# Optimization experiments

Hardware: AMD Instinct MI355X
Metric: run time of the kernel (lower is better)

Reference implementation:

```python
import jax, jax.numpy as jnp
import numpy as np
from math import comb

P, R, NC, SH = 2048, 32, 4, 3   # patches, resolution, degree+1 ctrl pts, max SH degree
N = P * R * R
NSH = (SH + 1) ** 2
EPS = 10.0


def _bernstein_basis():
    # Clamped knots [0]*(p+1)+[1]*(p+1) => B-spline basis == Bernstein polynomials.
    t = np.linspace(0.0, 1.0, R)
    bern = lambda p: np.stack([comb(p, k) * t**k * (1 - t)**(p - k) for k in range(p + 1)], -1)
    b3, b2, b1 = bern(3), bern(2), bern(1)
    db = 3.0 * (np.pad(b2, ((0, 0), (1, 0))) - np.pad(b2, ((0, 0), (0, 1))))
    ddb = 6.0 * (np.pad(b1, ((0, 0), (2, 0))) - 2.0 * np.pad(b1, ((0, 0), (1, 1))) + np.pad(b1, ((0, 0), (0, 2))))
    return b3.astype(np.float32), db.astype(np.float32), ddb.astype(np.float32)


def setup_inputs() -> dict:
    key = jax.random.key(0)
    ks = jax.random.split(key, 5)
    b, db, ddb = _bernstein_basis()
    tile = lambda a: jnp.asarray(np.broadcast_to(a, (P, R, NC)).copy())
    return {
        "control_points": jax.random.normal(ks[0], (P, NC, NC, 3), jnp.float32),
        "nurbs_weights": jax.random.uniform(ks[1], (P, NC, NC), jnp.float32, 0.5, 1.5),
        "sh_dc": jax.random.normal(ks[2], (P, NC, NC, 1, 3), jnp.float32),
        "sh_rest": jax.random.normal(ks[3], (P, NC, NC, NSH - 1, 3), jnp.float32) * 0.1,
        "scale_params": jax.random.uniform(ks[4], (P, 2), jnp.float32, 0.5, 1.5),
        "opacity": jnp.ones((N, 1), jnp.float32),
        "b_u": tile(b), "b_v": tile(b),
        "db_u": tile(db), "db_v": tile(db),
        "ddb_u": tile(ddb), "ddb_v": tile(ddb),
    }


def reference(control_points, nurbs_weights, sh_dc, sh_rest, scale_params, opacity,
              b_u, b_v, db_u, db_v, ddb_u, ddb_v):
    # NURBS rational denominator [P,R,R] -> [N,1]
    den = jnp.einsum('aik,ajl,akl->aij', b_u, b_v, nurbs_weights).reshape(-1, 1)
    den = jnp.where(den == 0, 1.0, den)
    wcp = control_points * nurbs_weights[..., None]        # weighted control points [P,4,4,3]
    surf = lambda Bu, Bv: jnp.einsum('aik,ajl,aklm->aijm', Bu, Bv, wcp).reshape(-1, 3) / den
    xyz = surf(b_u, b_v)
    dus = surf(db_u, b_v)
    dvs = surf(b_u, db_v)
    ddus = surf(ddb_u, b_v)
    ddvs = surf(b_u, ddb_v)

    # SH feature synthesis [N, 16, 3]
    sh_feat = jnp.concatenate([sh_dc, sh_rest], axis=-2).reshape(P, NC, NC, -1)
    shs = jnp.einsum('aik,ajl,aklm->aijm', b_u, b_v, sh_feat).reshape(-1, NSH, 3)

    # per-patch surface area (mean |du x dv| over the grid; param domain has unit area)
    cross = jnp.cross(dus, dvs)
    areas = jnp.linalg.norm(cross, axis=-1).reshape(P, R * R).mean(-1)          # [P]
    sp3 = jnp.concatenate([scale_params, jnp.full((P, 1), 1e-16, jnp.float32)], -1)
    scale_factors = jnp.repeat((areas[:, None] / R**2) * sp3, R * R, axis=0)    # [N,3]

    # torch uses F.normalize(..., p=1): L1 normalization
    normals = cross / jnp.maximum(jnp.abs(cross).sum(-1, keepdims=True), 1e-12)

    sx = (dus * dus).sum(-1) + EPS
    sy = (dvs * dvs).sum(-1) + EPS
    scaling_vec = jnp.stack([sx, sy, jnp.full_like(sx, EPS)], -1)
    curvature = jnp.stack([ddus.sum(-1), ddvs.sum(-1), jnp.ones_like(sx)], -1)
    # (sf*s).abs().sqrt().log() == 0.5*log|sf*s|
    scaling = 0.5 * jnp.log(jnp.abs(scale_factors * scaling_vec)) - jnp.log(jnp.abs(curvature) + EPS)

    # quaternion rotating up=[0,0,1] onto the (L2-unit) normal: q = normalize([1+dot, cross])
    n = normals / jnp.maximum(jnp.linalg.norm(normals, axis=-1, keepdims=True), 1e-12)
    w = 1.0 + n[:, 2:3]
    xyzq = jnp.stack([-n[:, 1], n[:, 0], jnp.zeros_like(n[:, 0])], -1)  # cross(up, n)
    q = jnp.concatenate([w, xyzq], -1)
    rotation = q / jnp.maximum(jnp.linalg.norm(q, axis=-1, keepdims=True), 1e-12)

    return (xyz, opacity, scaling, rotation, shs)
```

## Files before the change

### kernel.cpp

```cpp
#include <hip/hip_runtime.h>
#include <math.h>

#define NPATCH 2048
#define NPTS 1024
#define NTOT (NPATCH * NPTS)

using f4 = __attribute__((ext_vector_type(4))) float;

__device__ __forceinline__ void nt_store4(float* p, float a, float b, float c, float d) {
    f4 v = {a, b, c, d};
    __builtin_nontemporal_store(v, reinterpret_cast<f4*>(p));
}
__device__ __forceinline__ void nt_copy4(float* dst, const float* src) {
    f4 v = *reinterpret_cast<const f4*>(src);
    __builtin_nontemporal_store(v, reinterpret_cast<f4*>(dst));
}

__global__ __launch_bounds__(256) void area_kernel(
    const float* __restrict__ cp,
    const float* __restrict__ Wt,
    const float* __restrict__ b_u,
    const float* __restrict__ b_v,
    const float* __restrict__ db_u,
    const float* __restrict__ db_v,
    float* __restrict__ ws)
{
    const int a = blockIdx.x;
    const int t = threadIdx.x;

    __shared__ float s_W[16];
    __shared__ __align__(16) float s_wcp4[16][4];
    __shared__ __align__(16) float s_bu[32][4];
    __shared__ __align__(16) float s_bv[32][4];
    __shared__ __align__(16) float s_dbu[32][4];
    __shared__ __align__(16) float s_dbv[32][4];
    __shared__ __align__(16) float s_tB[128][4];
    __shared__ __align__(16) float s_tD[128][4];
    __shared__ __align__(16) float s_wB[128];
    __shared__ float s_red[4];

    if (t < 16) {
        const float w = Wt[a * 16 + t];
        s_W[t] = w;
        s_wcp4[t][0] = cp[a * 48 + t * 3 + 0] * w;
        s_wcp4[t][1] = cp[a * 48 + t * 3 + 1] * w;
        s_wcp4[t][2] = cp[a * 48 + t * 3 + 2] * w;
        s_wcp4[t][3] = 0.f;
    }
    if (t < 128) {
        s_bu [t >> 2][t & 3] = b_u [a * 128 + t];
        s_bv [t >> 2][t & 3] = b_v [a * 128 + t];
        s_dbu[t >> 2][t & 3] = db_u[a * 128 + t];
        s_dbv[t >> 2][t & 3] = db_v[a * 128 + t];
    }
    __syncthreads();

    if (t < 128) {
        const int i = t >> 2, l = t & 3;
        f4 acc = {0.f, 0.f, 0.f, 0.f};
        float wa = 0.f;
        #pragma unroll
        for (int k = 0; k < 4; ++k) {
            const float b = s_bu[i][k];
            acc += b * *reinterpret_cast<const f4*>(s_wcp4[k * 4 + l]);
            wa  += b * s_W[k * 4 + l];
        }
        *reinterpret_cast<f4*>(s_tB[t]) = acc;
        s_wB[t] = wa;
    } else {
        const int tt = t - 128;
        const int i = tt >> 2, l = tt & 3;
        f4 acc = {0.f, 0.f, 0.f, 0.f};
        #pragma unroll
        for (int k = 0; k < 4; ++k)
            acc += s_dbu[i][k] * *reinterpret_cast<const f4*>(s_wcp4[k * 4 + l]);
        *reinterpret_cast<f4*>(s_tD[tt]) = acc;
    }
    __syncthreads();

    const int j = t & 31;
    const f4 bv  = *reinterpret_cast<const f4*>(s_bv[j]);
    const f4 dbv = *reinterpret_cast<const f4*>(s_dbv[j]);

    float acc = 0.f;
    #pragma unroll
    for (int s2 = 0; s2 < 4; ++s2) {
        const int i = (t >> 5) + 8 * s2;
        const f4 tb0 = *reinterpret_cast<const f4*>(s_tB[i * 4 + 0]);
        const f4 tb1 = *reinterpret_cast<const f4*>(s_tB[i * 4 + 1]);
        const f4 tb2 = *reinterpret_cast<const f4*>(s_tB[i * 4 + 2]);
        const f4 tb3 = *reinterpret_cast<const f4*>(s_tB[i * 4 + 3]);
        const f4 td0 = *reinterpret_cast<const f4*>(s_tD[i * 4 + 0]);
        const f4 td1 = *reinterpret_cast<const f4*>(s_tD[i * 4 + 1]);
        const f4 td2 = *reinterpret_cast<const f4*>(s_tD[i * 4 + 2]);
        const f4 td3 = *reinterpret_cast<const f4*>(s_tD[i * 4 + 3]);
        const f4 wb  = *(reinterpret_cast<const f4*>(s_wB) + i);

        float den = bv.x * wb.x + bv.y * wb.y + bv.z * wb.z + bv.w * wb.w;
        if (den == 0.f) den = 1.f;
        const float inv = 1.0f / den;

        const f4 du = bv.x  * td0 + bv.y  * td1 + bv.z  * td2 + bv.w  * td3;
        const f4 dv = dbv.x * tb0 + dbv.y * tb1 + dbv.z * tb2 + dbv.w * tb3;

        const float cx = du.y * dv.z - du.z * dv.y;
        const float cy = du.z * dv.x - du.x * dv.z;
        const float cz = du.x * dv.y - du.y * dv.x;
        acc += sqrtf(cx * cx + cy * cy + cz * cz) * inv * inv;
    }

    #pragma unroll
    for (int off = 32; off > 0; off >>= 1)
        acc += __shfl_down(acc, off, 64);
    if ((t & 63) == 0) s_red[t >> 6] = acc;
    __syncthreads();
    if (t == 0) ws[a] = s_red[0] + s_red[1] + s_red[2] + s_red[3];
}

__global__ __launch_bounds__(256) void fused_kernel(
    const float* __restrict__ cp,
    const float* __restrict__ Wt,
    const float* __restrict__ sh_dc,
    const float* __restrict__ sh_rest,
    const float* __restrict__ spar,
    const float* __restrict__ opac,
    const float* __restrict__ b_u,
    const float* __restrict__ b_v,
    const float* __restrict__ db_u,
    const float* __restrict__ db_v,
    const float* __restrict__ ddb_u,
    const float* __restrict__ ddb_v,
    const float* __restrict__ ws,
    float* __restrict__ out)
{
    const int blk = blockIdx.x;
    const int a = blk >> 2, q = blk & 3;
    const int t = threadIdx.x;

    __shared__ float s_W[16];
    __shared__ __align__(16) float s_wcp4[16][4];
    __shared__ __align__(16) float g_bu[8][4];
    __shared__ __align__(16) float g_dbu[8][4];
    __shared__ __align__(16) float g_ddbu[8][4];
    __shared__ __align__(16) float g_bv[32][4];
    __shared__ __align__(16) float g_dbv[32][4];
    __shared__ __align__(16) float g_ddbv[32][4];
    __shared__ __align__(16) float s_tB[32][4];
    __shared__ __align__(16) float s_tD[32][4];
    __shared__ __align__(16) float s_tE[32][4];
    __shared__ __align__(16) float s_wB[32];
    __shared__ __align__(16) float s_sh[16][48];
    __shared__ __align__(16) float s_tmp[8 * 208];
    __shared__ __align__(16) float s_xyz[768];
    __shared__ __align__(16) float s_scl[768];

    if (t < 16) {
        const float w = Wt[a * 16 + t];
        s_W[t] = w;
        s_wcp4[t][0] = cp[a * 48 + t * 3 + 0] * w;
        s_wcp4[t][1] = cp[a * 48 + t * 3 + 1] * w;
        s_wcp4[t][2] = cp[a * 48 + t * 3 + 2] * w;
        s_wcp4[t][3] = 0.f;
    }
    if (t < 32) {
        g_bu  [t >> 2][t & 3] = b_u  [a * 128 + q * 32 + t];
        g_dbu [t >> 2][t & 3] = db_u [a * 128 + q * 32 + t];
        g_ddbu[t >> 2][t & 3] = ddb_u[a * 128 + q * 32 + t];
    }
    if (t < 128) {
        g_bv  [t >> 2][t & 3] = b_v  [a * 128 + t];
        g_dbv [t >> 2][t & 3] = db_v [a * 128 + t];
        g_ddbv[t >> 2][t & 3] = ddb_v[a * 128 + t];
    }
    for (int idx = t; idx < 768; idx += 256) {
        const int kl = idx / 48, c = idx - kl * 48;
        s_sh[kl][c] = (c < 3) ? sh_dc[a * 48 + kl * 3 + c]
                              : sh_rest[a * 720 + kl * 45 + (c - 3)];
    }
    __syncthreads();

    if (t < 32) {
        const int i = t >> 2, l = t & 3;
        f4 acc = {0.f, 0.f, 0.f, 0.f};
        float wa = 0.f;
        #pragma unroll
        for (int k = 0; k < 4; ++k) {
            const float b = g_bu[i][k];
            acc += b * *reinterpret_cast<const f4*>(s_wcp4[k * 4 + l]);
            wa  += b * s_W[k * 4 + l];
        }
        *reinterpret_cast<f4*>(s_tB[t]) = acc;
        s_wB[t] = wa;
    } else if (t < 64) {
        const int tt = t - 32, i = tt >> 2, l = tt & 3;
        f4 acc = {0.f, 0.f, 0.f, 0.f};
        #pragma unroll
        for (int k = 0; k < 4; ++k)
            acc += g_dbu[i][k] * *reinterpret_cast<const f4*>(s_wcp4[k * 4 + l]);
        *reinterpret_cast<f4*>(s_tD[tt]) = acc;
    } else if (t < 96) {
        const int tt = t - 64, i = tt >> 2, l = tt & 3;
        f4 acc = {0.f, 0.f, 0.f, 0.f};
        #pragma unroll
        for (int k = 0; k < 4; ++k)
            acc += g_ddbu[i][k] * *reinterpret_cast<const f4*>(s_wcp4[k * 4 + l]);
        *reinterpret_cast<f4*>(s_tE[tt]) = acc;
    }
    #pragma unroll
    for (int r = 0; r < 2; ++r) {
        const int e4 = t + r * 256;
        if (e4 < 384) {
            const int i = e4 / 48, rem = e4 - i * 48;
            const int l = rem / 12, cq = rem - l * 12;
            float ax = 0.f, ay = 0.f, az = 0.f, aw = 0.f;
            #pragma unroll
            for (int k = 0; k < 4; ++k) {
                const float w = g_bu[i][k];
                const float4 v = *reinterpret_cast<const float4*>(&s_sh[k * 4 + l][cq * 4]);
                ax += w * v.x; ay += w * v.y; az += w * v.z; aw += w * v.w;
            }
            *reinterpret_cast<float4*>(&s_tmp[i * 208 + l * 52 + cq * 4]) =
                make_float4(ax, ay, az, aw);
        }
    }
    __syncthreads();

    const long N3 = 3L * NTOT, N4 = 4L * NTOT, N7 = 7L * NTOT;
    const long n0 = (long)a * NPTS + q * 256;
    const long n  = n0 + t;

    {
        const int i = t >> 5, j = t & 31;
        const f4 bv   = *reinterpret_cast<const f4*>(g_bv[j]);
        const f4 dbv  = *reinterpret_cast<const f4*>(g_dbv[j]);
        const f4 ddbv = *reinterpret_cast<const f4*>(g_ddbv[j]);

        const f4 tb0 = *reinterpret_cast<const f4*>(s_tB[i * 4 + 0]);
        const f4 tb1 = *reinterpret_cast<const f4*>(s_tB[i * 4 + 1]);
        const f4 tb2 = *reinterpret_cast<const f4*>(s_tB[i * 4 + 2]);
        const f4 tb3 = *reinterpret_cast<const f4*>(s_tB[i * 4 + 3]);
        const f4 td0 = *reinterpret_cast<const f4*>(s_tD[i * 4 + 0]);
        const f4 td1 = *reinterpret_cast<const f4*>(s_tD[i * 4 + 1]);
        const f4 td2 = *reinterpret_cast<const f4*>(s_tD[i * 4 + 2]);
        const f4 td3 = *reinterpret_cast<const f4*>(s_tD[i * 4 + 3]);
        const f4 te0 = *reinterpret_cast<const f4*>(s_tE[i * 4 + 0]);
        const f4 te1 = *reinterpret_cast<const f4*>(s_tE[i * 4 + 1]);
        const f4 te2 = *reinterpret_cast<const f4*>(s_tE[i * 4 + 2]);
        const f4 te3 = *reinterpret_cast<const f4*>(s_tE[i * 4 + 3]);
        const f4 wb  = *(reinterpret_cast<const f4*>(s_wB) + i);

        float den = bv.x * wb.x + bv.y * wb.y + bv.z * wb.z + bv.w * wb.w;
        if (den == 0.f) den = 1.f;
        const float inv = 1.0f / den;

        const f4 xyz = bv.x  * tb0 + bv.y  * tb1 + bv.z  * tb2 + bv.w  * tb3;
        const f4 du  = bv.x  * td0 + bv.y  * td1 + bv.z  * td2 + bv.w  * td3;
        const f4 dv  = dbv.x * tb0 + dbv.y * tb1 + dbv.z * tb2 + dbv.w * tb3;
        const f4 eu  = bv.x  * te0 + bv.y  * te1 + bv.z  * te2 + bv.w  * te3;
        const f4 ev  = ddbv.x* tb0 + ddbv.y* tb1 + ddbv.z* tb2 + ddbv.w* tb3;

        const float x0 = xyz.x * inv, x1 = xyz.y * inv, x2 = xyz.z * inv;
        const float du0 = du.x * inv, du1 = du.y * inv, du2 = du.z * inv;
        const float dv0 = dv.x * inv, dv1 = dv.y * inv, dv2 = dv.z * inv;

        const float cx = du1 * dv2 - du2 * dv1;
        const float cy = du2 * dv0 - du0 * dv2;
        const float cz = du0 * dv1 - du1 * dv0;

        const float clen = sqrtf(cx * cx + cy * cy + cz * cz);
        const float rcl  = 1.0f / fmaxf(clen, 1e-20f);
        const float nx = cx * rcl, ny = cy * rcl, nz = cz * rcl;
        const float qw = 1.f + nz, qx = -ny, qy = nx;
        float qn = sqrtf(qw * qw + qx * qx + qy * qy);
        qn = fmaxf(qn, 1e-12f);
        const float rqn = 1.0f / qn;

        nt_store4(out + N7 + n * 4, qw * rqn, qx * rqn, qy * rqn, 0.f);

        if (t < 64)
            nt_copy4(out + N3 + n0 + 4 * t, opac + n0 + 4 * t);

        const float sx  = du0 * du0 + du1 * du1 + du2 * du2 + 10.f;
        const float sy  = dv0 * dv0 + dv1 * dv1 + dv2 * dv2 + 10.f;
        const float cvx = (eu.x + eu.y + eu.z) * inv;
        const float cvy = (ev.x + ev.y + ev.z) * inv;

        const float factor = ws[a] * (1.0f / 1024.0f) * (1.0f / 1024.0f);
        const float sp0 = spar[a * 2 + 0], sp1 = spar[a * 2 + 1];
        const float sf0 = factor * sp0;
        const float sf1 = factor * sp1;
        const float sf2 = factor * 1e-16f;

        s_xyz[t * 3 + 0] = x0;
        s_xyz[t * 3 + 1] = x1;
        s_xyz[t * 3 + 2] = x2;
        s_scl[t * 3 + 0] = 0.5f * __logf(fabsf(sf0 * sx)) - __logf(fabsf(cvx) + 10.f);
        s_scl[t * 3 + 1] = 0.5f * __logf(fabsf(sf1 * sy)) - __logf(fabsf(cvy) + 10.f);
        s_scl[t * 3 + 2] = 0.5f * __logf(fabsf(sf2 * 10.f)) - __logf(11.f);
    }
    __syncthreads();

    if (t < 192) {
        nt_copy4(out + n0 * 3 + 4 * t, s_xyz + 4 * t);
        nt_copy4(out + N4 + n0 * 3 + 4 * t, s_scl + 4 * t);
    }

    float* __restrict__ outp =
        out + 11L * NTOT + ((long)a * 12288 + q * 3072) * 4;

    #pragma unroll
    for (int k = 0; k < 12; ++k) {
        const unsigned f = t + (k << 8);
        const unsigned p = f / 12u;
        const unsigned c = f - p * 12u;
        const int i = p >> 5;
        const int j = p & 31;

        const float4 bv = *reinterpret_cast<const float4*>(g_bv[j]);
        const float* base = &s_tmp[i * 208 + c * 4];

        const float4 t0 = *reinterpret_cast<const float4*>(base + 0 * 52);
        const float4 t1 = *reinterpret_cast<const float4*>(base + 1 * 52);
        const float4 t2 = *reinterpret_cast<const float4*>(base + 2 * 52);
        const float4 t3 = *reinterpret_cast<const float4*>(base + 3 * 52);

        nt_store4(outp + f * 4,
            bv.x * t0.x + bv.y * t1.x + bv.z * t2.x + bv.w * t3.x,
            bv.x * t0.y + bv.y * t1.y + bv.z * t2.y + bv.w * t3.y,
            bv.x * t0.z + bv.y * t1.z + bv.z * t2.z + bv.w * t3.z,
            bv.x * t0.w + bv.y * t1.w + bv.z * t2.w + bv.w * t3.w);
    }
}

extern "C" void kernel_launch(void* const* d_in, const int* in_sizes, int n_in,
                              void* d_out, int out_size, void* d_ws, size_t ws_size,
                              hipStream_t stream) {
    const float* cp      = (const float*)d_in[0];
    const float* Wt      = (const float*)d_in[1];
    const float* sh_dc   = (const float*)d_in[2];
    const float* sh_rest = (const float*)d_in[3];
    const float* spar    = (const float*)d_in[4];
    const float* opac    = (const float*)d_in[5];
    const float* b_u     = (const float*)d_in[6];
    const float* b_v     = (const float*)d_in[7];
    const float* db_u    = (const float*)d_in[8];
    const float* db_v    = (const float*)d_in[9];
    const float* ddb_u   = (const float*)d_in[10];
    const float* ddb_v   = (const float*)d_in[11];
    float* out = (float*)d_out;
    float* ws  = (float*)d_ws;

    hipLaunchKernelGGL(area_kernel, dim3(NPATCH), dim3(256), 0, stream,
                       cp, Wt, b_u, b_v, db_u, db_v, ws);
    hipLaunchKernelGGL(fused_kernel, dim3(NPATCH * 4), dim3(256), 0, stream,
                       cp, Wt, sh_dc, sh_rest, spar, opac,
                       b_u, b_v, db_u, db_v, ddb_u, ddb_v, ws, out);
}
```

Baseline: 108.4 us.

## Fuse per-patch area reduction into main kernel, removing separate area pass

Drops the standalone area kernel and has each of the four blocks per patch recompute the full patch area reduction in shared memory before producing outputs. This removes a kernel launch and the workspace round-trip, but does the area computation four times per patch and adds two extra block barriers. It also swaps the shared-memory staged, coalesced float4 stores for xyz and scaling with per-thread strided scalar nontemporal stores.

```diff
diff --git a/kernel.cpp b/kernel.cpp
--- a/kernel.cpp
+++ b/kernel.cpp
@@ -15,109 +15,11 @@
     f4 v = *reinterpret_cast<const f4*>(src);
     __builtin_nontemporal_store(v, reinterpret_cast<f4*>(dst));
 }
-
-__global__ __launch_bounds__(256) void area_kernel(
-    const float* __restrict__ cp,
-    const float* __restrict__ Wt,
-    const float* __restrict__ b_u,
-    const float* __restrict__ b_v,
-    const float* __restrict__ db_u,
-    const float* __restrict__ db_v,
-    float* __restrict__ ws)
-{
-    const int a = blockIdx.x;
-    const int t = threadIdx.x;
-
-    __shared__ float s_W[16];
-    __shared__ __align__(16) float s_wcp4[16][4];
-    __shared__ __align__(16) float s_bu[32][4];
-    __shared__ __align__(16) float s_bv[32][4];
-    __shared__ __align__(16) float s_dbu[32][4];
-    __shared__ __align__(16) float s_dbv[32][4];
-    __shared__ __align__(16) float s_tB[128][4];
-    __shared__ __align__(16) float s_tD[128][4];
-    __shared__ __align__(16) float s_wB[128];
-    __shared__ float s_red[4];
-
-    if (t < 16) {
-        const float w = Wt[a * 16 + t];
-        s_W[t] = w;
-        s_wcp4[t][0] = cp[a * 48 + t * 3 + 0] * w;
-        s_wcp4[t][1] = cp[a * 48 + t * 3 + 1] * w;
-        s_wcp4[t][2] = cp[a * 48 + t * 3 + 2] * w;
-        s_wcp4[t][3] = 0.f;
-    }
-    if (t < 128) {
-        s_bu [t >> 2][t & 3] = b_u [a * 128 + t];
-        s_bv [t >> 2][t & 3] = b_v [a * 128 + t];
-        s_dbu[t >> 2][t & 3] = db_u[a * 128 + t];
-        s_dbv[t >> 2][t & 3] = db_v[a * 128 + t];
-    }
-    __syncthreads();
-
-    if (t < 128) {
-        const int i = t >> 2, l = t & 3;
-        f4 acc = {0.f, 0.f, 0.f, 0.f};
-        float wa = 0.f;
-        #pragma unroll
-        for (int k = 0; k < 4; ++k) {
-            const float b = s_bu[i][k];
-            acc += b * *reinterpret_cast<const f4*>(s_wcp4[k * 4 + l]);
-            wa  += b * s_W[k * 4 + l];
-        }
-        *reinterpret_cast<f4*>(s_tB[t]) = acc;
-        s_wB[t] = wa;
-    } else {
-        const int tt = t - 128;
-        const int i = tt >> 2, l = tt & 3;
-        f4 acc = {0.f, 0.f, 0.f, 0.f};
-        #pragma unroll
-        for (int k = 0; k < 4; ++k)
-            acc += s_dbu[i][k] * *reinterpret_cast<const f4*>(s_wcp4[k * 4 + l]);
-        *reinterpret_cast<f4*>(s_tD[tt]) = acc;
-    }
-    __syncthreads();
-
-    const int j = t & 31;
-    const f4 bv  = *reinterpret_cast<const f4*>(s_bv[j]);
-    const f4 dbv = *reinterpret_cast<const f4*>(s_dbv[j]);
-
-    float acc = 0.f;
-    #pragma unroll
-    for (int s2 = 0; s2 < 4; ++s2) {
-        const int i = (t >> 5) + 8 * s2;
-        const f4 tb0 = *reinterpret_cast<const f4*>(s_tB[i * 4 + 0]);
-        const f4 tb1 = *reinterpret_cast<const f4*>(s_tB[i * 4 + 1]);
-        const f4 tb2 = *reinterpret_cast<const f4*>(s_tB[i * 4 + 2]);
-        const f4 tb3 = *reinterpret_cast<const f4*>(s_tB[i * 4 + 3]);
-        const f4 td0 = *reinterpret_cast<const f4*>(s_tD[i * 4 + 0]);
-        const f4 td1 = *reinterpret_cast<const f4*>(s_tD[i * 4 + 1]);
-        const f4 td2 = *reinterpret_cast<const f4*>(s_tD[i * 4 + 2]);
-        const f4 td3 = *reinterpret_cast<const f4*>(s_tD[i * 4 + 3]);
-        const f4 wb  = *(reinterpret_cast<const f4*>(s_wB) + i);
-
-        float den = bv.x * wb.x + bv.y * wb.y + bv.z * wb.z + bv.w * wb.w;
-        if (den == 0.f) den = 1.f;
-        const float inv = 1.0f / den;
-
-        const f4 du = bv.x  * td0 + bv.y  * td1 + bv.z  * td2 + bv.w  * td3;
-        const f4 dv = dbv.x * tb0 + dbv.y * tb1 + dbv.z * tb2 + dbv.w * tb3;
-
-        const float cx = du.y * dv.z - du.z * dv.y;
-        const float cy = du.z * dv.x - du.x * dv.z;
-        const float cz = du.x * dv.y - du.y * dv.x;
-        acc += sqrtf(cx * cx + cy * cy + cz * cz) * inv * inv;
-    }
-
-    #pragma unroll
-    for (int off = 32; off > 0; off >>= 1)
-        acc += __shfl_down(acc, off, 64);
-    if ((t & 63) == 0) s_red[t >> 6] = acc;
-    __syncthreads();
-    if (t == 0) ws[a] = s_red[0] + s_red[1] + s_red[2] + s_red[3];
-}
-
-__global__ __launch_bounds__(256) void fused_kernel(
+__device__ __forceinline__ void nt_store1(float* p, float v) {
+    __builtin_nontemporal_store(v, p);
+}
+
+__global__ __launch_bounds__(256) void mega_kernel(
     const float* __restrict__ cp,
     const float* __restrict__ Wt,
     const float* __restrict__ sh_dc,
@@ -130,7 +32,6 @@
     const float* __restrict__ db_v,
     const float* __restrict__ ddb_u,
     const float* __restrict__ ddb_v,
-    const float* __restrict__ ws,
     float* __restrict__ out)
 {
     const int blk = blockIdx.x;
@@ -139,20 +40,20 @@
 
     __shared__ float s_W[16];
     __shared__ __align__(16) float s_wcp4[16][4];
-    __shared__ __align__(16) float g_bu[8][4];
-    __shared__ __align__(16) float g_dbu[8][4];
-    __shared__ __align__(16) float g_ddbu[8][4];
-    __shared__ __align__(16) float g_bv[32][4];
-    __shared__ __align__(16) float g_dbv[32][4];
-    __shared__ __align__(16) float g_ddbv[32][4];
-    __shared__ __align__(16) float s_tB[32][4];
-    __shared__ __align__(16) float s_tD[32][4];
+    __shared__ __align__(16) float s_bu[32][4];
+    __shared__ __align__(16) float s_dbu[32][4];
+    __shared__ __align__(16) float s_ddbu[8][4];
+    __shared__ __align__(16) float s_bv[32][4];
+    __shared__ __align__(16) float s_dbv[32][4];
+    __shared__ __align__(16) float s_ddbv[32][4];
+    __shared__ __align__(16) float s_tB[128][4];
+    __shared__ __align__(16) float s_tD[128][4];
     __shared__ __align__(16) float s_tE[32][4];
-    __shared__ __align__(16) float s_wB[32];
+    __shared__ __align__(16) float s_wB[128];
     __shared__ __align__(16) float s_sh[16][48];
     __shared__ __align__(16) float s_tmp[8 * 208];
-    __shared__ __align__(16) float s_xyz[768];
-    __shared__ __align__(16) float s_scl[768];
+    __shared__ float s_red[4];
+    __shared__ float s_area;
 
     if (t < 16) {
         const float w = Wt[a * 16 + t];
@@ -162,16 +63,15 @@
         s_wcp4[t][2] = cp[a * 48 + t * 3 + 2] * w;
         s_wcp4[t][3] = 0.f;
     }
-    if (t < 32) {
-        g_bu  [t >> 2][t & 3] = b_u  [a * 128 + q * 32 + t];
-        g_dbu [t >> 2][t & 3] = db_u [a * 128 + q * 32 + t];
-        g_ddbu[t >> 2][t & 3] = ddb_u[a * 128 + q * 32 + t];
-    }
     if (t < 128) {
-        g_bv  [t >> 2][t & 3] = b_v  [a * 128 + t];
-        g_dbv [t >> 2][t & 3] = db_v [a * 128 + t];
-        g_ddbv[t >> 2][t & 3] = ddb_v[a * 128 + t];
-    }
+        s_bu  [t >> 2][t & 3] = b_u  [a * 128 + t];
+        s_dbu [t >> 2][t & 3] = db_u [a * 128 + t];
+        s_bv  [t >> 2][t & 3] = b_v  [a * 128 + t];
+        s_dbv [t >> 2][t & 3] = db_v [a * 128 + t];
+        s_ddbv[t >> 2][t & 3] = ddb_v[a * 128 + t];
+    }
+    if (t < 32)
+        s_ddbu[t >> 2][t & 3] = ddb_u[a * 128 + q * 32 + t];
     for (int idx = t; idx < 768; idx += 256) {
         const int kl = idx / 48, c = idx - kl * 48;
         s_sh[kl][c] = (c < 3) ? sh_dc[a * 48 + kl * 3 + c]
@@ -179,32 +79,33 @@
     }
     __syncthreads();
 
-    if (t < 32) {
+    if (t < 128) {
         const int i = t >> 2, l = t & 3;
         f4 acc = {0.f, 0.f, 0.f, 0.f};
         float wa = 0.f;
         #pragma unroll
         for (int k = 0; k < 4; ++k) {
-            const float b = g_bu[i][k];
+            const float b = s_bu[i][k];
             acc += b * *reinterpret_cast<const f4*>(s_wcp4[k * 4 + l]);
             wa  += b * s_W[k * 4 + l];
         }
         *reinterpret_cast<f4*>(s_tB[t]) = acc;
         s_wB[t] = wa;
-    } else if (t < 64) {
-        const int tt = t - 32, i = tt >> 2, l = tt & 3;
+    } else {
+        const int tt = t - 128, i = tt >> 2, l = tt & 3;
         f4 acc = {0.f, 0.f, 0.f, 0.f};
         #pragma unroll
         for (int k = 0; k < 4; ++k)
-            acc += g_dbu[i][k] * *reinterpret_cast<const f4*>(s_wcp4[k * 4 + l]);
+            acc += s_dbu[i][k] * *reinterpret_cast<const f4*>(s_wcp4[k * 4 + l]);
         *reinterpret_cast<f4*>(s_tD[tt]) = acc;
-    } else if (t < 96) {
-        const int tt = t - 64, i = tt >> 2, l = tt & 3;
+    }
+    if (t < 32) {
+        const int i = t >> 2, l = t & 3;
         f4 acc = {0.f, 0.f, 0.f, 0.f};
         #pragma unroll
         for (int k = 0; k < 4; ++k)
-            acc += g_ddbu[i][k] * *reinterpret_cast<const f4*>(s_wcp4[k * 4 + l]);
-        *reinterpret_cast<f4*>(s_tE[tt]) = acc;
+            acc += s_ddbu[i][k] * *reinterpret_cast<const f4*>(s_wcp4[k * 4 + l]);
+        *reinterpret_cast<f4*>(s_tE[t]) = acc;
     }
     #pragma unroll
     for (int r = 0; r < 2; ++r) {
@@ -215,7 +116,7 @@
             float ax = 0.f, ay = 0.f, az = 0.f, aw = 0.f;
             #pragma unroll
             for (int k = 0; k < 4; ++k) {
-                const float w = g_bu[i][k];
+                const float w = s_bu[q * 8 + i][k];
                 const float4 v = *reinterpret_cast<const float4*>(&s_sh[k * 4 + l][cq * 4]);
                 ax += w * v.x; ay += w * v.y; az += w * v.z; aw += w * v.w;
             }
@@ -225,39 +126,77 @@
     }
     __syncthreads();
 
+    const int j = t & 31;
+    const f4 bvJ  = *reinterpret_cast<const f4*>(s_bv[j]);
+    const f4 dbvJ = *reinterpret_cast<const f4*>(s_dbv[j]);
+    {
+        float acc = 0.f;
+        #pragma unroll
+        for (int s2 = 0; s2 < 4; ++s2) {
+            const int i = (t >> 5) + 8 * s2;
+            const f4 tb0 = *reinterpret_cast<const f4*>(s_tB[i * 4 + 0]);
+            const f4 tb1 = *reinterpret_cast<const f4*>(s_tB[i * 4 + 1]);
+            const f4 tb2 = *reinterpret_cast<const f4*>(s_tB[i * 4 + 2]);
+            const f4 tb3 = *reinterpret_cast<const f4*>(s_tB[i * 4 + 3]);
+            const f4 td0 = *reinterpret_cast<const f4*>(s_tD[i * 4 + 0]);
+            const f4 td1 = *reinterpret_cast<const f4*>(s_tD[i * 4 + 1]);
+            const f4 td2 = *reinterpret_cast<const f4*>(s_tD[i * 4 + 2]);
+            const f4 td3 = *reinterpret_cast<const f4*>(s_tD[i * 4 + 3]);
+            const f4 wb  = *(reinterpret_cast<const f4*>(s_wB) + i);
+
+            float den = bvJ.x * wb.x + bvJ.y * wb.y + bvJ.z * wb.z + bvJ.w * wb.w;
+            if (den == 0.f) den = 1.f;
+            const float inv = 1.0f / den;
+
+            const f4 du = bvJ.x  * td0 + bvJ.y  * td1 + bvJ.z  * td2 + bvJ.w  * td3;
+            const f4 dv = dbvJ.x * tb0 + dbvJ.y * tb1 + dbvJ.z * tb2 + dbvJ.w * tb3;
+
+            const float cx = du.y * dv.z - du.z * dv.y;
+            const float cy = du.z * dv.x - du.x * dv.z;
+            const float cz = du.x * dv.y - du.y * dv.x;
+            acc += sqrtf(cx * cx + cy * cy + cz * cz) * inv * inv;
+        }
+        #pragma unroll
+        for (int off = 32; off > 0; off >>= 1)
+            acc += __shfl_down(acc, off, 64);
+        if ((t & 63) == 0) s_red[t >> 6] = acc;
+    }
+    __syncthreads();
+    if (t == 0) s_area = s_red[0] + s_red[1] + s_red[2] + s_red[3];
+    __syncthreads();
+
     const long N3 = 3L * NTOT, N4 = 4L * NTOT, N7 = 7L * NTOT;
     const long n0 = (long)a * NPTS + q * 256;
     const long n  = n0 + t;
 
     {
-        const int i = t >> 5, j = t & 31;
-        const f4 bv   = *reinterpret_cast<const f4*>(g_bv[j]);
-        const f4 dbv  = *reinterpret_cast<const f4*>(g_dbv[j]);
-        const f4 ddbv = *reinterpret_cast<const f4*>(g_ddbv[j]);
-
-        const f4 tb0 = *reinterpret_cast<const f4*>(s_tB[i * 4 + 0]);
-        const f4 tb1 = *reinterpret_cast<const f4*>(s_tB[i * 4 + 1]);
-        const f4 tb2 = *reinterpret_cast<const f4*>(s_tB[i * 4 + 2]);
-        const f4 tb3 = *reinterpret_cast<const f4*>(s_tB[i * 4 + 3]);
-        const f4 td0 = *reinterpret_cast<const f4*>(s_tD[i * 4 + 0]);
-        const f4 td1 = *reinterpret_cast<const f4*>(s_tD[i * 4 + 1]);
-        const f4 td2 = *reinterpret_cast<const f4*>(s_tD[i * 4 + 2]);
-        const f4 td3 = *reinterpret_cast<const f4*>(s_tD[i * 4 + 3]);
-        const f4 te0 = *reinterpret_cast<const f4*>(s_tE[i * 4 + 0]);
-        const f4 te1 = *reinterpret_cast<const f4*>(s_tE[i * 4 + 1]);
-        const f4 te2 = *reinterpret_cast<const f4*>(s_tE[i * 4 + 2]);
-        const f4 te3 = *reinterpret_cast<const f4*>(s_tE[i * 4 + 3]);
-        const f4 wb  = *(reinterpret_cast<const f4*>(s_wB) + i);
-
-        float den = bv.x * wb.x + bv.y * wb.y + bv.z * wb.z + bv.w * wb.w;
+        const int gi = q * 8 + (t >> 5);
+        const f4 ddbvJ = *reinterpret_cast<const f4*>(s_ddbv[j]);
+
+        const f4 tb0 = *reinterpret_cast<const f4*>(s_tB[gi * 4 + 0]);
+        const f4 tb1 = *reinterpret_cast<const f4*>(s_tB[gi * 4 + 1]);
+        const f4 tb2 = *reinterpret_cast<const f4*>(s_tB[gi * 4 + 2]);
+        const f4 tb3 = *reinterpret_cast<const f4*>(s_tB[gi * 4 + 3]);
+        const f4 td0 = *reinterpret_cast<const f4*>(s_tD[gi * 4 + 0]);
+        const f4 td1 = *reinterpret_cast<const f4*>(s_tD[gi * 4 + 1]);
+        const f4 td2 = *reinterpret_cast<const f4*>(s_tD[gi * 4 + 2]);
+        const f4 td3 = *reinterpret_cast<const f4*>(s_tD[gi * 4 + 3]);
+        const int il = t >> 5;
+        const f4 te0 = *reinterpret_cast<const f4*>(s_tE[il * 4 + 0]);
+        const f4 te1 = *reinterpret_cast<const f4*>(s_tE[il * 4 + 1]);
+        const f4 te2 = *reinterpret_cast<const f4*>(s_tE[il * 4 + 2]);
+        const f4 te3 = *reinterpret_cast<const f4*>(s_tE[il * 4 + 3]);
+        const f4 wb  = *(reinterpret_cast<const f4*>(s_wB) + gi);
+
+        float den = bvJ.x * wb.x + bvJ.y * wb.y + bvJ.z * wb.z + bvJ.w * wb.w;
         if (den == 0.f) den = 1.f;
         const float inv = 1.0f / den;
 
-        const f4 xyz = bv.x  * tb0 + bv.y  * tb1 + bv.z  * tb2 + bv.w  * tb3;
-        const f4 du  = bv.x  * td0 + bv.y  * td1 + bv.z  * td2 + bv.w  * td3;
-        const f4 dv  = dbv.x * tb0 + dbv.y * tb1 + dbv.z * tb2 + dbv.w * tb3;
-        const f4 eu  = bv.x  * te0 + bv.y  * te1 + bv.z  * te2 + bv.w  * te3;
-        const f4 ev  = ddbv.x* tb0 + ddbv.y* tb1 + ddbv.z* tb2 + ddbv.w* tb3;
+        const f4 xyz = bvJ.x  * tb0 + bvJ.y  * tb1 + bvJ.z  * tb2 + bvJ.w  * tb3;
+        const f4 du  = bvJ.x  * td0 + bvJ.y  * td1 + bvJ.z  * td2 + bvJ.w  * td3;
+        const f4 dv  = dbvJ.x * tb0 + dbvJ.y * tb1 + dbvJ.z * tb2 + dbvJ.w * tb3;
+        const f4 eu  = bvJ.x  * te0 + bvJ.y  * te1 + bvJ.z  * te2 + bvJ.w  * te3;
+        const f4 ev  = ddbvJ.x* tb0 + ddbvJ.y* tb1 + ddbvJ.z* tb2 + ddbvJ.w* tb3;
 
         const float x0 = xyz.x * inv, x1 = xyz.y * inv, x2 = xyz.z * inv;
         const float du0 = du.x * inv, du1 = du.y * inv, du2 = du.z * inv;
@@ -276,6 +215,9 @@
         const float rqn = 1.0f / qn;
 
         nt_store4(out + N7 + n * 4, qw * rqn, qx * rqn, qy * rqn, 0.f);
+        nt_store1(out + n * 3 + 0, x0);
+        nt_store1(out + n * 3 + 1, x1);
+        nt_store1(out + n * 3 + 2, x2);
 
         if (t < 64)
             nt_copy4(out + N3 + n0 + 4 * t, opac + n0 + 4 * t);
@@ -285,24 +227,18 @@
         const float cvx = (eu.x + eu.y + eu.z) * inv;
         const float cvy = (ev.x + ev.y + ev.z) * inv;
 
-        const float factor = ws[a] * (1.0f / 1024.0f) * (1.0f / 1024.0f);
+        const float factor = s_area * (1.0f / 1024.0f) * (1.0f / 1024.0f);
         const float sp0 = spar[a * 2 + 0], sp1 = spar[a * 2 + 1];
         const float sf0 = factor * sp0;
         const float sf1 = factor * sp1;
         const float sf2 = factor * 1e-16f;
 
-        s_xyz[t * 3 + 0] = x0;
-        s_xyz[t * 3 + 1] = x1;
-        s_xyz[t * 3 + 2] = x2;
-        s_scl[t * 3 + 0] = 0.5f * __logf(fabsf(sf0 * sx)) - __logf(fabsf(cvx) + 10.f);
-        s_scl[t * 3 + 1] = 0.5f * __logf(fabsf(sf1 * sy)) - __logf(fabsf(cvy) + 10.f);
-        s_scl[t * 3 + 2] = 0.5f * __logf(fabsf(sf2 * 10.f)) - __logf(11.f);
-    }
-    __syncthreads();
-
-    if (t < 192) {
-        nt_copy4(out + n0 * 3 + 4 * t, s_xyz + 4 * t);
-        nt_copy4(out + N4 + n0 * 3 + 4 * t, s_scl + 4 * t);
+        nt_store1(out + N4 + n * 3 + 0,
+                  0.5f * __logf(fabsf(sf0 * sx)) - __logf(fabsf(cvx) + 10.f));
+        nt_store1(out + N4 + n * 3 + 1,
+                  0.5f * __logf(fabsf(sf1 * sy)) - __logf(fabsf(cvy) + 10.f));
+        nt_store1(out + N4 + n * 3 + 2,
+                  0.5f * __logf(fabsf(sf2 * 10.f)) - __logf(11.f));
     }
 
     float* __restrict__ outp =
@@ -314,9 +250,9 @@
         const unsigned p = f / 12u;
         const unsigned c = f - p * 12u;
         const int i = p >> 5;
-        const int j = p & 31;
-
-        const float4 bv = *reinterpret_cast<const float4*>(g_bv[j]);
+        const int jj = p & 31;
+
+        const float4 bv = *reinterpret_cast<const float4*>(s_bv[jj]);
         const float* base = &s_tmp[i * 208 + c * 4];
 
         const float4 t0 = *reinterpret_cast<const float4*>(base + 0 * 52);
@@ -348,11 +284,8 @@
     const float* ddb_u   = (const float*)d_in[10];
     const float* ddb_v   = (const float*)d_in[11];
     float* out = (float*)d_out;
-    float* ws  = (float*)d_ws;
-
-    hipLaunchKernelGGL(area_kernel, dim3(NPATCH), dim3(256), 0, stream,
-                       cp, Wt, b_u, b_v, db_u, db_v, ws);
-    hipLaunchKernelGGL(fused_kernel, dim3(NPATCH * 4), dim3(256), 0, stream,
+
+    hipLaunchKernelGGL(mega_kernel, dim3(NPATCH * 4), dim3(256), 0, stream,
                        cp, Wt, sh_dc, sh_rest, spar, opac,
-                       b_u, b_v, db_u, db_v, ddb_u, ddb_v, ws, out);
-}
+                       b_u, b_v, db_u, db_v, ddb_u, ddb_v, out);
+}
```

New measurement: 103.6 us. 4.5% less time.
